# Performance work log

Measured on AMD Instinct MI355X. Metric: run time of the kernel, lower is better.

Reference implementation:

```python
import jax, jax.numpy as jnp
import numpy as np

NSITES, NUP, NDN, BATCH = 256, 128, 128, 4096

def setup_inputs() -> dict:
    key = jax.random.key(0)
    k1, k2, k3, k4, k5 = jax.random.split(key, 5)
    phi_up = jax.random.normal(k1, (NSITES, NUP), dtype=jnp.float32)
    phi_dn = jax.random.normal(k2, (NSITES, NDN), dtype=jnp.float32)
    nfmodes = 2 * NSITES
    v = jax.random.normal(k3, (nfmodes, nfmodes), dtype=jnp.float32) / nfmodes
    # occupation: exactly NUP ones in first NSITES slots, NDN ones in last NSITES
    base_up = jnp.concatenate([jnp.ones(NUP, jnp.int32), jnp.zeros(NSITES - NUP, jnp.int32)])
    base_dn = jnp.concatenate([jnp.ones(NDN, jnp.int32), jnp.zeros(NSITES - NDN, jnp.int32)])
    n_up = jax.vmap(lambda k: jax.random.permutation(k, base_up))(jax.random.split(k4, BATCH))
    n_dn = jax.vmap(lambda k: jax.random.permutation(k, base_dn))(jax.random.split(k5, BATCH))
    n = jnp.concatenate([n_up, n_dn], axis=1)  # [B, 2*nsites]
    return {"n": n, "phi_up": phi_up, "phi_dn": phi_dn, "v": v}

def reference(n, phi_up, phi_dn, v):
    nsites, nup = phi_up.shape
    nf = n.astype(phi_up.dtype)                       # [B, 2*nsites]
    # Jastrow log factor: -0.5 * n @ v @ n  (sign is +1)
    log_j = -0.5 * jnp.einsum('bi,ij,bj->b', nf, v, nf)
    # fermion_idx: sorted indices of occupied modes, split by spin sector.
    # stable argsort of -n gives occupied indices in ascending order.
    idx_up = jnp.argsort(-n[:, :nsites], axis=1)[:, :nup]          # [B, nup]
    idx_dn = jnp.argsort(-n[:, nsites:], axis=1)[:, :phi_dn.shape[1]]
    M_up = phi_up[idx_up]                             # [B, nup, nup]
    M_dn = phi_dn[idx_dn]                             # [B, ndn, ndn]
    sign_up, logabs_up = jnp.linalg.slogdet(M_up)
    sign_dn, logabs_dn = jnp.linalg.slogdet(M_dn)
    sign = sign_up * sign_dn                          # jastrow sign is ones
    logabs = log_j + logabs_up + logabs_dn
    return jnp.stack([sign, logabs], axis=0)          # [2, B]
```

## Files before the change

### kernel.cpp

```cpp
#include <hip/hip_runtime.h>
#include <hip/hip_bf16.h>

#define NSITES 256
#define NM 128
#define NMODES 512

typedef unsigned long long u64;
typedef unsigned int u32;

#define REP8(M)    M(0) M(1) M(2) M(3) M(4) M(5) M(6) M(7)
#define REP8P(M,P) M(0,P) M(1,P) M(2,P) M(3,P) M(4,P) M(5,P) M(6,P) M(7,P)

template<int CTRL>
__device__ __forceinline__ int dpp_imax(int x) {
  const int y = __builtin_amdgcn_update_dpp(x, x, CTRL, 0xF, 0xF, false);
  return x > y ? x : y;
}
__device__ __forceinline__ int wave_imax_key(int x) {
  x = dpp_imax<0x128>(x);
  x = dpp_imax<0x124>(x);
  x = dpp_imax<0x122>(x);
  x = dpp_imax<0x121>(x);
  x = dpp_imax<0x142>(x);
  x = dpp_imax<0x143>(x);
  return __builtin_amdgcn_readfirstlane(__builtin_amdgcn_readlane(x, 63));
}
__device__ __forceinline__ float rl2(float x1, float x2, int p) {
  const int v1 = __builtin_amdgcn_readlane(__float_as_int(x1), p & 63);
  const int v2 = __builtin_amdgcn_readlane(__float_as_int(x2), p & 63);
  return __int_as_float(p < 64 ? v1 : v2);
}
__device__ __forceinline__ float bperm(int byteidx, float v) {
  return __int_as_float(__builtin_amdgcn_ds_bpermute(byteidx, __float_as_int(v)));
}

__global__ __launch_bounds__(256, 2) void lu_kernel(
    const int* __restrict__ n, const float* __restrict__ phi_up,
    const float* __restrict__ phi_dn, float* __restrict__ ws, int B)
{
  __shared__ int occ[NSITES];
  __shared__ int wcnt[4];
  __shared__ float colbuf[2][NM];
  __shared__ int ipiv[NM];

  const int t = threadIdx.x;
  const int ty = t & 15, tx = t >> 4;
  const int lane = t & 63, wv = t >> 6;
  const int bs = blockIdx.x;
  const int b = bs >> 1, spin = bs & 1;
  const int* nn = n + b * NMODES + spin * NSITES;
  const float* phi = spin ? phi_dn : phi_up;

  {
    int v = nn[t];
    u64 m = __ballot(v != 0);
    if (lane == 0) wcnt[wv] = __popcll(m);
    __syncthreads();
    int off = 0;
    for (int w = 0; w < wv; ++w) off += wcnt[w];
    if (v) occ[off + __popcll(m & ((1ull << lane) - 1))] = t;
    __syncthreads();
  }

  float a[8][8];
#define GATH(II) { const float* pr_ = phi + occ[(II)*16 + ty] * NM; \
  a[II][0] = pr_[0*16+tx]; a[II][1] = pr_[1*16+tx]; \
  a[II][2] = pr_[2*16+tx]; a[II][3] = pr_[3*16+tx]; \
  a[II][4] = pr_[4*16+tx]; a[II][5] = pr_[5*16+tx]; \
  a[II][6] = pr_[6*16+tx]; a[II][7] = pr_[7*16+tx]; }
  REP8(GATH)
#undef GATH

#define PUBP(II, DST) DST[(II)*16 + ty] = a[II][0];
  if (tx == 0) { float* d_ = &colbuf[0][0]; REP8P(PUBP, d_) }
  if (tx == 1) { float* d_ = &colbuf[1][0]; REP8P(PUBP, d_) }
#undef PUBP
  __syncthreads();

  float c1 = colbuf[0][lane];
  float c2 = colbuf[0][lane + 64];
  int r1 = 0, r2 = 0;
  float l2sum = 0.f;
  int sb = 0;
  const int bidx0 = (ty) << 2;
  const int bidx1 = (16 + ty) << 2;
  const int bidx2 = (32 + ty) << 2;
  const int bidx3 = (48 + ty) << 2;

  for (int k = 0; k < NM; ++k) {
    const int cur = k & 1;
    __syncthreads();

    const float d1 = colbuf[cur ^ 1][lane];
    const float d2 = colbuf[cur ^ 1][lane + 64];

    const int ka1 = r1 ? 0 : ((__float_as_int(c1) & 0x7FFFFF80) | lane);
    const int ka2 = r2 ? 0 : ((__float_as_int(c2) & 0x7FFFFF80) | (lane + 64));
    const int key = wave_imax_key(ka1 > ka2 ? ka1 : ka2);
    const int p = key & 127;
    const float pivv = rl2(c1, c2, p);
    const float rpiv = __builtin_amdgcn_rcpf(pivv);
    r1 |= (p == lane);
    r2 |= (p == lane + 64);
    const float m1 = r1 ? 0.f : c1 * rpiv;
    const float m2 = r2 ? 0.f : c2 * rpiv;
    if (t == 0) ipiv[k] = p;
    l2sum += __log2f(fabsf(pivv));
    sb ^= (int)(__float_as_uint(pivv) >> 31);

    if (k < NM - 1) {
      float w0, w1, w2, w3, w4, w5, w6, w7;
      switch (p >> 4) {
#define CPW(II) case II: w0=a[II][0]; w1=a[II][1]; w2=a[II][2]; w3=a[II][3]; \
  w4=a[II][4]; w5=a[II][5]; w6=a[II][6]; w7=a[II][7]; break;
        REP8(CPW)
#undef CPW
      }
      const int idxP = ((lane & 0x30) | (p & 15)) << 2;

      float mI[8];
      mI[0] = bperm(bidx0, m1); mI[1] = bperm(bidx1, m1);
      mI[2] = bperm(bidx2, m1); mI[3] = bperm(bidx3, m1);
      mI[4] = bperm(bidx0, m2); mI[5] = bperm(bidx1, m2);
      mI[6] = bperm(bidx2, m2); mI[7] = bperm(bidx3, m2);

      const int T = (k + 1) >> 4;
      float pr[8];
#define PRE(JJ, KB) if ((JJ) >= (KB)) pr[JJ] = bperm(idxP, w##JJ);
#define UPDROW(II, KB) { \
  if (0 >= (KB)) a[II][0] = fmaf(-mI[II], pr[0], a[II][0]); \
  if (1 >= (KB)) a[II][1] = fmaf(-mI[II], pr[1], a[II][1]); \
  if (2 >= (KB)) a[II][2] = fmaf(-mI[II], pr[2], a[II][2]); \
  if (3 >= (KB)) a[II][3] = fmaf(-mI[II], pr[3], a[II][3]); \
  if (4 >= (KB)) a[II][4] = fmaf(-mI[II], pr[4], a[II][4]); \
  if (5 >= (KB)) a[II][5] = fmaf(-mI[II], pr[5], a[II][5]); \
  if (6 >= (KB)) a[II][6] = fmaf(-mI[II], pr[6], a[II][6]); \
  if (7 >= (KB)) a[II][7] = fmaf(-mI[II], pr[7], a[II][7]); }
#define LUCASE(KB) case KB: { REP8P(PRE, KB) REP8P(UPDROW, KB) } break;
      switch (T) {
        REP8(LUCASE)
      }
#undef LUCASE
#undef UPDROW
#undef PRE

      const float ud = rl2(d1, d2, p);
      c1 = fmaf(-m1, ud, d1);
      c2 = fmaf(-m2, ud, d2);

      if (k < NM - 2) {
        const int cn = k + 2;
        if (tx == (cn & 15)) {
          float* dst = &colbuf[cur][0];
          switch (cn >> 4) {
#define PUBJ(JJ) case JJ: \
  dst[0*16+ty]=a[0][JJ]; dst[1*16+ty]=a[1][JJ]; dst[2*16+ty]=a[2][JJ]; dst[3*16+ty]=a[3][JJ]; \
  dst[4*16+ty]=a[4][JJ]; dst[5*16+ty]=a[5][JJ]; dst[6*16+ty]=a[6][JJ]; dst[7*16+ty]=a[7][JJ]; break;
            REP8(PUBJ)
#undef PUBJ
          }
        }
      }
    }
  }

  __syncthreads();
  int inv = 0;
  if (t < NM) {
    const int my = ipiv[t];
    for (int l = t + 1; l < NM; ++l) inv += (my > ipiv[l]) ? 1 : 0;
  }
  const u64 bal = __ballot((t < NM) && (inv & 1));
  if (lane == 0) wcnt[wv] = __popcll(bal);
  __syncthreads();

  if (t == 0) {
    const int par = (wcnt[0] + wcnt[1] + wcnt[2] + wcnt[3]) & 1;
    const int s = (sb ^ par) & 1;
    ws[B + spin * B + b] = l2sum * 0.6931471805599453f;
    ws[3 * B + spin * B + b] = s ? -1.f : 1.f;
  }
}

__global__ __launch_bounds__(256) void jastrow_kernel(
    const int* __restrict__ n, const float* __restrict__ v,
    float* __restrict__ ws, int B)
{
  __shared__ int occ[256];
  __shared__ float nf[NMODES];
  __shared__ int wcnt[8];
  __shared__ float red[256];
  const int t = threadIdx.x, b = blockIdx.x;
  const int lane = t & 63, wv = t >> 6;
  const int* nn = n + b * NMODES;
  int v0 = nn[t], v1 = nn[256 + t];
  nf[t] = (float)v0;
  nf[256 + t] = (float)v1;
  u64 m0 = __ballot(v0 != 0), m1 = __ballot(v1 != 0);
  if (lane == 0) { wcnt[wv] = __popcll(m0); wcnt[4 + wv] = __popcll(m1); }
  __syncthreads();
  int off0 = 0;
  for (int w = 0; w < wv; ++w) off0 += wcnt[w];
  int base1 = wcnt[0] + wcnt[1] + wcnt[2] + wcnt[3];
  int off1 = base1;
  for (int w = 0; w < wv; ++w) off1 += wcnt[4 + w];
  if (v0) occ[off0 + __popcll(m0 & ((1ull << lane) - 1))] = t;
  if (v1) occ[off1 + __popcll(m1 & ((1ull << lane) - 1))] = 256 + t;
  __syncthreads();

  float acc = 0.f;
  for (int r = wv * 64; r < wv * 64 + 64; ++r) {
    const float* row = v + occ[r] * NMODES;
#pragma unroll
    for (int cc = 0; cc < 8; ++cc) {
      int c = cc * 64 + lane;
      acc += row[c] * nf[c];
    }
  }
  red[t] = acc;
  __syncthreads();
  for (int s = 128; s >= 1; s >>= 1) {
    if (t < s) red[t] += red[t + s];
    __syncthreads();
  }
  if (t == 0) ws[b] = -0.5f * red[0];
}

__global__ void finalize_kernel(const float* __restrict__ ws,
                                float* __restrict__ out, int B)
{
  int b = blockIdx.x * 256 + threadIdx.x;
  if (b < B) {
    float lj = ws[b];
    float la_u = ws[B + b], la_d = ws[2 * B + b];
    float s_u = ws[3 * B + b], s_d = ws[4 * B + b];
    out[b] = s_u * s_d;
    out[B + b] = lj + la_u + la_d;
  }
}

extern "C" void kernel_launch(void* const* d_in, const int* in_sizes, int n_in,
                              void* d_out, int out_size, void* d_ws, size_t ws_size,
                              hipStream_t stream) {
  const int* n = (const int*)d_in[0];
  const float* phi_up = (const float*)d_in[1];
  const float* phi_dn = (const float*)d_in[2];
  const float* v = (const float*)d_in[3];
  float* out = (float*)d_out;
  float* ws = (float*)d_ws;
  const int B = in_sizes[0] / NMODES;

  jastrow_kernel<<<B, 256, 0, stream>>>(n, v, ws, B);
  lu_kernel<<<2 * B, 256, 0, stream>>>(n, phi_up, phi_dn, ws, B);
  finalize_kernel<<<(B + 255) / 256, 256, 0, stream>>>(ws, out, B);
}
```

Measured before the change: 2.039 ms.

## Factor both spin LU decompositions in one block with interleaved pivot steps

Each block now holds both the up and down 128x128 matrices in registers and runs their LU eliminations interleaved. One barrier per step then serves two independent factorizations, and the two dependency chains can hide each other's latency. The pivot row is now staged through shared memory by the owning thread row instead of being broadcast with ds_bpermute. In exchange, register pressure roughly doubles (128 accumulator floats per thread), which risks spills or lower occupancy under launch_bounds(256,2), and only half as many blocks are launched.

```diff
diff --git a/kernel.cpp b/kernel.cpp
--- a/kernel.cpp
+++ b/kernel.cpp
@@ -23,7 +23,7 @@
   x = dpp_imax<0x121>(x);
   x = dpp_imax<0x142>(x);
   x = dpp_imax<0x143>(x);
-  return __builtin_amdgcn_readfirstlane(__builtin_amdgcn_readlane(x, 63));
+  return __builtin_amdgcn_readlane(x, 63);
 }
 __device__ __forceinline__ float rl2(float x1, float x2, int p) {
   const int v1 = __builtin_amdgcn_readlane(__float_as_int(x1), p & 63);
@@ -38,124 +38,159 @@
     const int* __restrict__ n, const float* __restrict__ phi_up,
     const float* __restrict__ phi_dn, float* __restrict__ ws, int B)
 {
-  __shared__ int occ[NSITES];
-  __shared__ int wcnt[4];
-  __shared__ float colbuf[2][NM];
-  __shared__ int ipiv[NM];
+  __shared__ int occ[256];
+  __shared__ int wcnt[8];
+  __shared__ float colbufA[2][NM], colbufB[2][NM];
+  __shared__ float rowPA[2][NM], rowPB[2][NM];
+  __shared__ int ipivA[NM], ipivB[NM];
 
   const int t = threadIdx.x;
-  const int ty = t & 15, tx = t >> 4;
+  const int tx = t & 15, ty = t >> 4;
   const int lane = t & 63, wv = t >> 6;
-  const int bs = blockIdx.x;
-  const int b = bs >> 1, spin = bs & 1;
-  const int* nn = n + b * NMODES + spin * NSITES;
-  const float* phi = spin ? phi_dn : phi_up;
+  const int b = blockIdx.x;
+  const int* nn = n + b * NMODES;
 
   {
-    int v = nn[t];
-    u64 m = __ballot(v != 0);
-    if (lane == 0) wcnt[wv] = __popcll(m);
+    const int v0 = nn[t];
+    const int v1 = nn[256 + t];
+    const u64 m0 = __ballot(v0 != 0), m1 = __ballot(v1 != 0);
+    if (lane == 0) { wcnt[wv] = __popcll(m0); wcnt[4 + wv] = __popcll(m1); }
     __syncthreads();
-    int off = 0;
-    for (int w = 0; w < wv; ++w) off += wcnt[w];
-    if (v) occ[off + __popcll(m & ((1ull << lane) - 1))] = t;
+    int off0 = 0, off1 = 128;
+    for (int w = 0; w < wv; ++w) { off0 += wcnt[w]; off1 += wcnt[4 + w]; }
+    if (v0) occ[off0 + __popcll(m0 & ((1ull << lane) - 1))] = t;
+    if (v1) occ[off1 + __popcll(m1 & ((1ull << lane) - 1))] = t;
     __syncthreads();
   }
 
-  float a[8][8];
-#define GATH(II) { const float* pr_ = phi + occ[(II)*16 + ty] * NM; \
-  a[II][0] = pr_[0*16+tx]; a[II][1] = pr_[1*16+tx]; \
-  a[II][2] = pr_[2*16+tx]; a[II][3] = pr_[3*16+tx]; \
-  a[II][4] = pr_[4*16+tx]; a[II][5] = pr_[5*16+tx]; \
-  a[II][6] = pr_[6*16+tx]; a[II][7] = pr_[7*16+tx]; }
-  REP8(GATH)
-#undef GATH
-
-#define PUBP(II, DST) DST[(II)*16 + ty] = a[II][0];
-  if (tx == 0) { float* d_ = &colbuf[0][0]; REP8P(PUBP, d_) }
-  if (tx == 1) { float* d_ = &colbuf[1][0]; REP8P(PUBP, d_) }
-#undef PUBP
-  __syncthreads();
-
-  float c1 = colbuf[0][lane];
-  float c2 = colbuf[0][lane + 64];
-  int r1 = 0, r2 = 0;
-  float l2sum = 0.f;
-  int sb = 0;
+  float aA[8][8], aB[8][8];
+#define GATHA(II) { const float* g_ = phi_up + occ[(II)*16 + ty] * NM; \
+  aA[II][0]=g_[0*16+tx]; aA[II][1]=g_[1*16+tx]; aA[II][2]=g_[2*16+tx]; aA[II][3]=g_[3*16+tx]; \
+  aA[II][4]=g_[4*16+tx]; aA[II][5]=g_[5*16+tx]; aA[II][6]=g_[6*16+tx]; aA[II][7]=g_[7*16+tx]; }
+#define GATHB(II) { const float* g_ = phi_dn + occ[128 + (II)*16 + ty] * NM; \
+  aB[II][0]=g_[0*16+tx]; aB[II][1]=g_[1*16+tx]; aB[II][2]=g_[2*16+tx]; aB[II][3]=g_[3*16+tx]; \
+  aB[II][4]=g_[4*16+tx]; aB[II][5]=g_[5*16+tx]; aB[II][6]=g_[6*16+tx]; aB[II][7]=g_[7*16+tx]; }
+  REP8(GATHA)
+  REP8(GATHB)
+#undef GATHA
+#undef GATHB
+
+#define PUB0(II) { colbufA[0][(II)*16+ty] = aA[II][0]; colbufB[0][(II)*16+ty] = aB[II][0]; }
+#define PUB1(II) { colbufA[1][(II)*16+ty] = aA[II][0]; colbufB[1][(II)*16+ty] = aB[II][0]; }
+  if (tx == 0) { REP8(PUB0) }
+  if (tx == 1) { REP8(PUB1) }
+#undef PUB0
+#undef PUB1
+  __syncthreads();
+
+  float c1A = colbufA[0][lane], c2A = colbufA[0][lane + 64];
+  float c1B = colbufB[0][lane], c2B = colbufB[0][lane + 64];
+  int r1A = 0, r2A = 0, r1B = 0, r2B = 0;
+  float l2sumA = 0.f, l2sumB = 0.f;
+  int sbA = 0, sbB = 0;
   const int bidx0 = (ty) << 2;
   const int bidx1 = (16 + ty) << 2;
   const int bidx2 = (32 + ty) << 2;
   const int bidx3 = (48 + ty) << 2;
 
+#define SRP_CASE(II, ARR) case II: \
+  dst_[0*16+tx]=ARR[II][0]; dst_[1*16+tx]=ARR[II][1]; dst_[2*16+tx]=ARR[II][2]; dst_[3*16+tx]=ARR[II][3]; \
+  dst_[4*16+tx]=ARR[II][4]; dst_[5*16+tx]=ARR[II][5]; dst_[6*16+tx]=ARR[II][6]; dst_[7*16+tx]=ARR[II][7]; break;
+
+#define DO_AMAX(X) { \
+  const int ka1 = r1##X ? 0 : ((__float_as_int(c1##X) & 0x7FFFFF80) | lane); \
+  const int ka2 = r2##X ? 0 : ((__float_as_int(c2##X) & 0x7FFFFF80) | (lane + 64)); \
+  key##X = wave_imax_key(ka1 > ka2 ? ka1 : ka2); \
+}
+#define DO_MULT(X) { \
+  p##X = key##X & 127; \
+  pivv##X = rl2(c1##X, c2##X, p##X); \
+  const float rp_ = __builtin_amdgcn_rcpf(pivv##X); \
+  r1##X |= (p##X == lane); \
+  r2##X |= (p##X == lane + 64); \
+  m1##X = r1##X ? 0.f : c1##X * rp_; \
+  m2##X = r2##X ? 0.f : c2##X * rp_; \
+}
+#define DO_STAGE(X) { \
+  if (k < NM - 1 && ty == (p##X & 15)) { \
+    float* dst_ = &rowP##X[cur][0]; \
+    switch (p##X >> 4) { REP8P(SRP_CASE, a##X) } \
+  } \
+  if (wv == 0) { \
+    if (lane == 0) ipiv##X[k] = p##X; \
+    l2sum##X += __log2f(fabsf(pivv##X)); \
+    sb##X ^= (int)(__float_as_uint(pivv##X) >> 31); \
+  } \
+}
+
   for (int k = 0; k < NM; ++k) {
     const int cur = k & 1;
+    int keyA, keyB, pA, pB;
+    float pivvA, pivvB, m1A, m2A, m1B, m2B;
+
+    DO_AMAX(A)
+    DO_AMAX(B)
+    DO_MULT(A)
+    DO_MULT(B)
+    DO_STAGE(A)
+    DO_STAGE(B)
+
     __syncthreads();
 
-    const float d1 = colbuf[cur ^ 1][lane];
-    const float d2 = colbuf[cur ^ 1][lane + 64];
-
-    const int ka1 = r1 ? 0 : ((__float_as_int(c1) & 0x7FFFFF80) | lane);
-    const int ka2 = r2 ? 0 : ((__float_as_int(c2) & 0x7FFFFF80) | (lane + 64));
-    const int key = wave_imax_key(ka1 > ka2 ? ka1 : ka2);
-    const int p = key & 127;
-    const float pivv = rl2(c1, c2, p);
-    const float rpiv = __builtin_amdgcn_rcpf(pivv);
-    r1 |= (p == lane);
-    r2 |= (p == lane + 64);
-    const float m1 = r1 ? 0.f : c1 * rpiv;
-    const float m2 = r2 ? 0.f : c2 * rpiv;
-    if (t == 0) ipiv[k] = p;
-    l2sum += __log2f(fabsf(pivv));
-    sb ^= (int)(__float_as_uint(pivv) >> 31);
-
     if (k < NM - 1) {
-      float w0, w1, w2, w3, w4, w5, w6, w7;
-      switch (p >> 4) {
-#define CPW(II) case II: w0=a[II][0]; w1=a[II][1]; w2=a[II][2]; w3=a[II][3]; \
-  w4=a[II][4]; w5=a[II][5]; w6=a[II][6]; w7=a[II][7]; break;
-        REP8(CPW)
-#undef CPW
-      }
-      const int idxP = ((lane & 0x30) | (p & 15)) << 2;
-
-      float mI[8];
-      mI[0] = bperm(bidx0, m1); mI[1] = bperm(bidx1, m1);
-      mI[2] = bperm(bidx2, m1); mI[3] = bperm(bidx3, m1);
-      mI[4] = bperm(bidx0, m2); mI[5] = bperm(bidx1, m2);
-      mI[6] = bperm(bidx2, m2); mI[7] = bperm(bidx3, m2);
-
+      const float dA1 = colbufA[cur ^ 1][lane], dA2 = colbufA[cur ^ 1][lane + 64];
+      const float dB1 = colbufB[cur ^ 1][lane], dB2 = colbufB[cur ^ 1][lane + 64];
+
+      float mIA[8], mIB[8];
+      mIA[0] = bperm(bidx0, m1A); mIA[1] = bperm(bidx1, m1A);
+      mIA[2] = bperm(bidx2, m1A); mIA[3] = bperm(bidx3, m1A);
+      mIA[4] = bperm(bidx0, m2A); mIA[5] = bperm(bidx1, m2A);
+      mIA[6] = bperm(bidx2, m2A); mIA[7] = bperm(bidx3, m2A);
+      mIB[0] = bperm(bidx0, m1B); mIB[1] = bperm(bidx1, m1B);
+      mIB[2] = bperm(bidx2, m1B); mIB[3] = bperm(bidx3, m1B);
+      mIB[4] = bperm(bidx0, m2B); mIB[5] = bperm(bidx1, m2B);
+      mIB[6] = bperm(bidx2, m2B); mIB[7] = bperm(bidx3, m2B);
+
+      const float* rPA_ = &rowPA[cur][0];
+      const float* rPB_ = &rowPB[cur][0];
+      float prA[8], prB[8];
       const int T = (k + 1) >> 4;
-      float pr[8];
-#define PRE(JJ, KB) if ((JJ) >= (KB)) pr[JJ] = bperm(idxP, w##JJ);
-#define UPDROW(II, KB) { \
-  if (0 >= (KB)) a[II][0] = fmaf(-mI[II], pr[0], a[II][0]); \
-  if (1 >= (KB)) a[II][1] = fmaf(-mI[II], pr[1], a[II][1]); \
-  if (2 >= (KB)) a[II][2] = fmaf(-mI[II], pr[2], a[II][2]); \
-  if (3 >= (KB)) a[II][3] = fmaf(-mI[II], pr[3], a[II][3]); \
-  if (4 >= (KB)) a[II][4] = fmaf(-mI[II], pr[4], a[II][4]); \
-  if (5 >= (KB)) a[II][5] = fmaf(-mI[II], pr[5], a[II][5]); \
-  if (6 >= (KB)) a[II][6] = fmaf(-mI[II], pr[6], a[II][6]); \
-  if (7 >= (KB)) a[II][7] = fmaf(-mI[II], pr[7], a[II][7]); }
-#define LUCASE(KB) case KB: { REP8P(PRE, KB) REP8P(UPDROW, KB) } break;
+#define PRE2(JJ, KB) if ((JJ) >= (KB)) { prA[JJ] = rPA_[(JJ)*16 + tx]; prB[JJ] = rPB_[(JJ)*16 + tx]; }
+#define UPD2(II, KB) { \
+  if (0 >= (KB)) { aA[II][0]=fmaf(-mIA[II],prA[0],aA[II][0]); aB[II][0]=fmaf(-mIB[II],prB[0],aB[II][0]); } \
+  if (1 >= (KB)) { aA[II][1]=fmaf(-mIA[II],prA[1],aA[II][1]); aB[II][1]=fmaf(-mIB[II],prB[1],aB[II][1]); } \
+  if (2 >= (KB)) { aA[II][2]=fmaf(-mIA[II],prA[2],aA[II][2]); aB[II][2]=fmaf(-mIB[II],prB[2],aB[II][2]); } \
+  if (3 >= (KB)) { aA[II][3]=fmaf(-mIA[II],prA[3],aA[II][3]); aB[II][3]=fmaf(-mIB[II],prB[3],aB[II][3]); } \
+  if (4 >= (KB)) { aA[II][4]=fmaf(-mIA[II],prA[4],aA[II][4]); aB[II][4]=fmaf(-mIB[II],prB[4],aB[II][4]); } \
+  if (5 >= (KB)) { aA[II][5]=fmaf(-mIA[II],prA[5],aA[II][5]); aB[II][5]=fmaf(-mIB[II],prB[5],aB[II][5]); } \
+  if (6 >= (KB)) { aA[II][6]=fmaf(-mIA[II],prA[6],aA[II][6]); aB[II][6]=fmaf(-mIB[II],prB[6],aB[II][6]); } \
+  if (7 >= (KB)) { aA[II][7]=fmaf(-mIA[II],prA[7],aA[II][7]); aB[II][7]=fmaf(-mIB[II],prB[7],aB[II][7]); } }
+#define LUCASE(KB) case KB: { REP8P(PRE2, KB) REP8P(UPD2, KB) } break;
       switch (T) {
         REP8(LUCASE)
       }
 #undef LUCASE
-#undef UPDROW
-#undef PRE
-
-      const float ud = rl2(d1, d2, p);
-      c1 = fmaf(-m1, ud, d1);
-      c2 = fmaf(-m2, ud, d2);
+#undef UPD2
+#undef PRE2
+
+      const float udA = rl2(dA1, dA2, pA);
+      c1A = fmaf(-m1A, udA, dA1);
+      c2A = fmaf(-m2A, udA, dA2);
+      const float udB = rl2(dB1, dB2, pB);
+      c1B = fmaf(-m1B, udB, dB1);
+      c2B = fmaf(-m2B, udB, dB2);
 
       if (k < NM - 2) {
         const int cn = k + 2;
         if (tx == (cn & 15)) {
-          float* dst = &colbuf[cur][0];
+          float* cbA_ = &colbufA[cur][0];
+          float* cbB_ = &colbufB[cur][0];
           switch (cn >> 4) {
 #define PUBJ(JJ) case JJ: \
-  dst[0*16+ty]=a[0][JJ]; dst[1*16+ty]=a[1][JJ]; dst[2*16+ty]=a[2][JJ]; dst[3*16+ty]=a[3][JJ]; \
-  dst[4*16+ty]=a[4][JJ]; dst[5*16+ty]=a[5][JJ]; dst[6*16+ty]=a[6][JJ]; dst[7*16+ty]=a[7][JJ]; break;
+  cbA_[0*16+ty]=aA[0][JJ]; cbA_[1*16+ty]=aA[1][JJ]; cbA_[2*16+ty]=aA[2][JJ]; cbA_[3*16+ty]=aA[3][JJ]; \
+  cbA_[4*16+ty]=aA[4][JJ]; cbA_[5*16+ty]=aA[5][JJ]; cbA_[6*16+ty]=aA[6][JJ]; cbA_[7*16+ty]=aA[7][JJ]; \
+  cbB_[0*16+ty]=aB[0][JJ]; cbB_[1*16+ty]=aB[1][JJ]; cbB_[2*16+ty]=aB[2][JJ]; cbB_[3*16+ty]=aB[3][JJ]; \
+  cbB_[4*16+ty]=aB[4][JJ]; cbB_[5*16+ty]=aB[5][JJ]; cbB_[6*16+ty]=aB[6][JJ]; cbB_[7*16+ty]=aB[7][JJ]; break;
             REP8(PUBJ)
 #undef PUBJ
           }
@@ -163,22 +198,31 @@
       }
     }
   }
-
-  __syncthreads();
-  int inv = 0;
-  if (t < NM) {
-    const int my = ipiv[t];
-    for (int l = t + 1; l < NM; ++l) inv += (my > ipiv[l]) ? 1 : 0;
-  }
-  const u64 bal = __ballot((t < NM) && (inv & 1));
-  if (lane == 0) wcnt[wv] = __popcll(bal);
+#undef DO_STAGE
+#undef DO_MULT
+#undef DO_AMAX
+#undef SRP_CASE
+
+  __syncthreads();
+  {
+    const int* ip = (t < 128) ? ipivA : ipivB;
+    const int tt = t & 127;
+    const int my = ip[tt];
+    int inv = 0;
+    for (int l = tt + 1; l < NM; ++l) inv += (my > ip[l]) ? 1 : 0;
+    const u64 bal = __ballot(inv & 1);
+    if (lane == 0) wcnt[wv] = __popcll(bal);
+  }
   __syncthreads();
 
   if (t == 0) {
-    const int par = (wcnt[0] + wcnt[1] + wcnt[2] + wcnt[3]) & 1;
-    const int s = (sb ^ par) & 1;
-    ws[B + spin * B + b] = l2sum * 0.6931471805599453f;
-    ws[3 * B + spin * B + b] = s ? -1.f : 1.f;
+    const int parA = (wcnt[0] + wcnt[1]) & 1;
+    const int parB = (wcnt[2] + wcnt[3]) & 1;
+    const float LN2 = 0.6931471805599453f;
+    ws[B + 0 * B + b] = l2sumA * LN2;
+    ws[B + 1 * B + b] = l2sumB * LN2;
+    ws[3 * B + 0 * B + b] = ((sbA ^ parA) & 1) ? -1.f : 1.f;
+    ws[3 * B + 1 * B + b] = ((sbB ^ parB) & 1) ? -1.f : 1.f;
   }
 }
 
@@ -251,6 +295,6 @@
   const int B = in_sizes[0] / NMODES;
 
   jastrow_kernel<<<B, 256, 0, stream>>>(n, v, ws, B);
-  lu_kernel<<<2 * B, 256, 0, stream>>>(n, phi_up, phi_dn, ws, B);
+  lu_kernel<<<B, 256, 0, stream>>>(n, phi_up, phi_dn, ws, B);
   finalize_kernel<<<(B + 255) / 256, 256, 0, stream>>>(ws, out, B);
 }
```

Measured after the change: 2.662 ms. 30.6% more time.
